# Kernel optimization log

Hardware: AMD Instinct MI355X
Metric: run time of the kernel (lower is better)

The kernel has to match this reference:

```python
import jax, jax.numpy as jnp
import numpy as np
import math

D_MODEL = 1024
EMB_DIM = 33
BANDS = (EMB_DIM - 1) // 2  # 16
FAST_DECAY_PCT = 0.3
SLOW_DECAY_PCT = 1.5
TARGET = 0.01
MOD_SHIFT = 0.0


def setup_inputs() -> dict:
    key = jax.random.key(0)
    ks = jax.random.split(key, 11)
    B, L = 2, 8192
    order = 64
    return {
        "x": jax.random.normal(ks[0], (B, D_MODEL, L), dtype=jnp.float32),
        "L": L,
        "lin_in_w": jax.random.normal(ks[1], (EMB_DIM, order), dtype=jnp.float32) * 0.1,
        "lin_in_b": jax.random.normal(ks[2], (order,), dtype=jnp.float32) * 0.1,
        "freq": jnp.ones((1, order), dtype=jnp.float32),  # Sin freq param, w=1
        "inner1_w": jax.random.normal(ks[3], (order, order), dtype=jnp.float32) * 0.1,
        "inner1_b": jax.random.normal(ks[4], (order,), dtype=jnp.float32) * 0.1,
        "inner2_w": jax.random.normal(ks[5], (order, order), dtype=jnp.float32) * 0.1,
        "inner2_b": jax.random.normal(ks[6], (order,), dtype=jnp.float32) * 0.1,
        "out_w": jax.random.normal(ks[7], (order, D_MODEL), dtype=jnp.float32) * 0.1,
        "D": jax.random.normal(ks[8], (D_MODEL,), dtype=jnp.float32),
    }


def _pos_emb(L):
    # ComplexExponentialPositionalEmbedding buffers (constants)
    t = jnp.linspace(0.0, 1.0, L, dtype=jnp.float32)[:, None]          # [L, 1]
    t_rescaled = jnp.linspace(0.0, L - 1, L, dtype=jnp.float32)[:, None]
    w = 2.0 * math.pi * t_rescaled / L                                  # [L, 1]
    f = jnp.linspace(1e-4, BANDS - 1, BANDS, dtype=jnp.float32)[None, :]
    theta = f * w                                                       # [L, bands]
    # z = exp(-1j * theta): real = cos(theta), imag = -sin(theta)
    z = jnp.concatenate([t, jnp.cos(theta), -jnp.sin(theta)], axis=-1)  # [L, emb_dim]
    return z, t


def reference(x, L, lin_in_w, lin_in_b, freq, inner1_w, inner1_b, inner2_w, inner2_b, out_w, D):
    # --- implicit filter MLP (Sin activations share one freq param) ---
    z, t = _pos_emb(L)
    h = jnp.sin(freq * (z @ lin_in_w + lin_in_b))
    h = jnp.sin(freq * (h @ inner1_w + inner1_b))
    h = jnp.sin(freq * (h @ inner2_w + inner2_b))
    h = h @ out_w                                                # [L, d_model]

    # --- exponential modulation ---
    max_decay = math.log(TARGET) / FAST_DECAY_PCT
    min_decay = math.log(TARGET) / SLOW_DECAY_PCT
    deltas = jnp.linspace(min_decay, max_decay, D_MODEL, dtype=jnp.float32)[None, :]
    decay = jnp.exp(-t * jnp.abs(deltas))                        # [L, d_model]
    h = h * (decay + MOD_SHIFT)

    k = h.T                                                      # [d_model, L]

    # --- FFT causal long convolution ---
    fft_size = 2 * L
    k_f = jnp.fft.rfft(k, n=fft_size) / fft_size                 # [d_model, L+1]
    u_f = jnp.fft.rfft(x, n=fft_size)                            # [B, d_model, L+1]
    y = jnp.fft.irfft(u_f * k_f, n=fft_size, norm="forward")[..., :L]
    out = y + x * D[:, None]                                     # bias skip connection
    return out.astype(x.dtype)
```

## Files before the change

### kernel.cpp

```cpp
#include <hip/hip_runtime.h>

#define D_MODEL 1024
#define LSEQ    8192
#define NC      8192
#define PI_F    3.14159265358979323846f
#define TWO_PI_OVER_N 3.8349519697141029e-4f
#define R2F  0.70710678118654752440f
#define C18F 0.92387953251128675613f
#define S18F 0.38268343236508977173f

__device__ __forceinline__ int sw(int p) { return p ^ ((p >> 7) & 15) ^ ((p >> 3) & 7); }
__device__ __forceinline__ int rev13(int x) { return (int)(__brev((unsigned)x) >> 19); }
__device__ __forceinline__ float2 cmulf(float2 a, float2 b) {
    return make_float2(a.x*b.x - a.y*b.y, a.x*b.y + a.y*b.x);
}

__device__ __forceinline__ void bf_dif(float2& a, float2& b, float c, float s) {
    float tx = a.x - b.x, ty = a.y - b.y;
    a.x += b.x; a.y += b.y;
    b.x = tx*c - ty*s; b.y = tx*s + ty*c;
}
__device__ __forceinline__ void bf_dif1(float2& a, float2& b) {
    float tx = a.x - b.x, ty = a.y - b.y;
    a.x += b.x; a.y += b.y;
    b.x = tx; b.y = ty;
}
__device__ __forceinline__ void bf_dif_mi(float2& a, float2& b) {
    float tx = a.x - b.x, ty = a.y - b.y;
    a.x += b.x; a.y += b.y;
    b.x = ty; b.y = -tx;
}
__device__ __forceinline__ void bf_dit(float2& a, float2& b, float c, float s) {
    float bx = b.x*c - b.y*s, by = b.x*s + b.y*c;
    b.x = a.x - bx; b.y = a.y - by;
    a.x += bx; a.y += by;
}
__device__ __forceinline__ void bf_dit1(float2& a, float2& b) {
    float bx = b.x, by = b.y;
    b.x = a.x - bx; b.y = a.y - by;
    a.x += bx; a.y += by;
}
__device__ __forceinline__ void bf_dit_pi(float2& a, float2& b) {
    float bx = -b.y, by = b.x;
    b.x = a.x - bx; b.y = a.y - by;
    a.x += bx; a.y += by;
}
__device__ __forceinline__ void bf_dit_a(float2& a, float2 b, float c, float s) {
    a.x += b.x*c - b.y*s; a.y += b.x*s + b.y*c;
}

template<int H>
__device__ __forceinline__ void fwd_pass8(float2* s, int tid) {
    const float astep = -PI_F / (float)H;
    #pragma unroll 1
    for (int gg = 0; gg < 4; ++gg) {
        int gi   = tid + gg * 256;
        int q    = gi & (H/4 - 1);
        int base = (gi - q) * 8 + q;
        float2 v[8];
        #pragma unroll
        for (int m = 0; m < 8; ++m) v[m] = s[sw(base + m*(H/4))];
        float a = astep * (float)q;
        float c1,s1,c2,s2,c4,s4;
        __sincosf(a,     &s1, &c1);
        __sincosf(a+a,   &s2, &c2);
        __sincosf(4.f*a, &s4, &c4);
        bf_dif(v[0], v[4], c1, s1);
        bf_dif(v[1], v[5], R2F*(c1+s1), R2F*(s1-c1));
        bf_dif(v[2], v[6], s1, -c1);
        bf_dif(v[3], v[7], R2F*(s1-c1), -R2F*(c1+s1));
        bf_dif(v[0], v[2], c2, s2);  bf_dif(v[4], v[6], c2, s2);
        bf_dif(v[1], v[3], s2, -c2); bf_dif(v[5], v[7], s2, -c2);
        bf_dif(v[0], v[1], c4, s4); bf_dif(v[2], v[3], c4, s4);
        bf_dif(v[4], v[5], c4, s4); bf_dif(v[6], v[7], c4, s4);
        #pragma unroll
        for (int m = 0; m < 8; ++m) s[sw(base + m*(H/4))] = v[m];
    }
}

__device__ __forceinline__ void dif16(float2* v) {
    bf_dif1 (v[0], v[8]);
    bf_dif  (v[1], v[9],   C18F, -S18F);
    bf_dif  (v[2], v[10],  R2F,  -R2F);
    bf_dif  (v[3], v[11],  S18F, -C18F);
    bf_dif_mi(v[4], v[12]);
    bf_dif  (v[5], v[13], -S18F, -C18F);
    bf_dif  (v[6], v[14], -R2F,  -R2F);
    bf_dif  (v[7], v[15], -C18F, -S18F);
    bf_dif1 (v[0], v[4]);              bf_dif1 (v[8],  v[12]);
    bf_dif  (v[1], v[5],  R2F, -R2F);  bf_dif  (v[9],  v[13],  R2F, -R2F);
    bf_dif_mi(v[2], v[6]);             bf_dif_mi(v[10], v[14]);
    bf_dif  (v[3], v[7], -R2F, -R2F);  bf_dif  (v[11], v[15], -R2F, -R2F);
    bf_dif1 (v[0], v[2]); bf_dif1 (v[4], v[6]); bf_dif1 (v[8], v[10]); bf_dif1 (v[12], v[14]);
    bf_dif_mi(v[1], v[3]); bf_dif_mi(v[5], v[7]); bf_dif_mi(v[9], v[11]); bf_dif_mi(v[13], v[15]);
    bf_dif1(v[0], v[1]); bf_dif1(v[2], v[3]);  bf_dif1(v[4], v[5]);  bf_dif1(v[6], v[7]);
    bf_dif1(v[8], v[9]); bf_dif1(v[10],v[11]); bf_dif1(v[12],v[13]); bf_dif1(v[14],v[15]);
}

__device__ __forceinline__ void fwd_fft(float2* s, int tid, const float2* __restrict__ g) {
    {
        const float astep = -PI_F / 4096.0f;
        #pragma unroll 1
        for (int gg = 0; gg < 4; ++gg) {
            int q = tid + gg * 256;
            float2 v[8];
            #pragma unroll
            for (int m = 0; m < 4; ++m) v[m] = g[q + m*1024];
            float a = astep * (float)q;
            float c1,s1,c2,s2,c4,s4;
            __sincosf(a,     &s1, &c1);
            __sincosf(a+a,   &s2, &c2);
            __sincosf(4.f*a, &s4, &c4);
            float wc, ws;
            wc = c1;            ws = s1;             v[4] = make_float2(v[0].x*wc - v[0].y*ws, v[0].x*ws + v[0].y*wc);
            wc = R2F*(c1+s1);   ws = R2F*(s1-c1);    v[5] = make_float2(v[1].x*wc - v[1].y*ws, v[1].x*ws + v[1].y*wc);
            wc = s1;            ws = -c1;            v[6] = make_float2(v[2].x*wc - v[2].y*ws, v[2].x*ws + v[2].y*wc);
            wc = R2F*(s1-c1);   ws = -R2F*(c1+s1);   v[7] = make_float2(v[3].x*wc - v[3].y*ws, v[3].x*ws + v[3].y*wc);
            bf_dif(v[0], v[2], c2, s2);  bf_dif(v[4], v[6], c2, s2);
            bf_dif(v[1], v[3], s2, -c2); bf_dif(v[5], v[7], s2, -c2);
            bf_dif(v[0], v[1], c4, s4); bf_dif(v[2], v[3], c4, s4);
            bf_dif(v[4], v[5], c4, s4); bf_dif(v[6], v[7], c4, s4);
            #pragma unroll
            for (int m = 0; m < 8; ++m) s[sw(q + m*1024)] = v[m];
        }
    }
    __syncthreads();
    fwd_pass8<512>(s, tid);
    __syncthreads();
    fwd_pass8<64>(s, tid);
    __syncthreads();
    #pragma unroll 1
    for (int gg = 0; gg < 2; ++gg) {
        int base = (tid + gg * 256) << 4;
        float2 v[16];
        #pragma unroll
        for (int m = 0; m < 16; ++m) v[m] = s[sw(base + m)];
        dif16(v);
        #pragma unroll
        for (int m = 0; m < 16; ++m) s[sw(base + m)] = v[m];
    }
}

__device__ __forceinline__ void dit16(float2* v) {
    bf_dit1(v[0], v[1]); bf_dit1(v[2], v[3]);  bf_dit1(v[4], v[5]);  bf_dit1(v[6], v[7]);
    bf_dit1(v[8], v[9]); bf_dit1(v[10],v[11]); bf_dit1(v[12],v[13]); bf_dit1(v[14],v[15]);
    bf_dit1 (v[0], v[2]); bf_dit_pi(v[1], v[3]);
    bf_dit1 (v[4], v[6]); bf_dit_pi(v[5], v[7]);
    bf_dit1 (v[8], v[10]); bf_dit_pi(v[9], v[11]);
    bf_dit1 (v[12],v[14]); bf_dit_pi(v[13],v[15]);
    bf_dit1 (v[0], v[4]);             bf_dit1 (v[8],  v[12]);
    bf_dit  (v[1], v[5],  R2F, R2F);  bf_dit  (v[9],  v[13],  R2F, R2F);
    bf_dit_pi(v[2], v[6]);            bf_dit_pi(v[10], v[14]);
    bf_dit  (v[3], v[7], -R2F, R2F);  bf_dit  (v[11], v[15], -R2F, R2F);
    bf_dit1 (v[0], v[8]);
    bf_dit  (v[1], v[9],   C18F, S18F);
    bf_dit  (v[2], v[10],  R2F,  R2F);
    bf_dit  (v[3], v[11],  S18F, C18F);
    bf_dit_pi(v[4], v[12]);
    bf_dit  (v[5], v[13], -S18F, C18F);
    bf_dit  (v[6], v[14], -R2F,  R2F);
    bf_dit  (v[7], v[15], -C18F, S18F);
}

template<int H>
__device__ __forceinline__ void inv_pass8(float2* s, int tid) {
    const float bstep = PI_F / (float)(4*H);
    #pragma unroll 1
    for (int gg = 0; gg < 4; ++gg) {
        int gi   = tid + gg * 256;
        int q    = gi & (H - 1);
        int base = (gi - q) * 8 + q;
        float2 v[8];
        #pragma unroll
        for (int m = 0; m < 8; ++m) v[m] = s[sw(base + m*H)];
        float bb = bstep * (float)q;
        float cb,sb,c2,s2,c4,s4;
        __sincosf(bb,      &sb, &cb);
        __sincosf(bb+bb,   &s2, &c2);
        __sincosf(4.f*bb,  &s4, &c4);
        bf_dit(v[0],v[1],c4,s4); bf_dit(v[2],v[3],c4,s4);
        bf_dit(v[4],v[5],c4,s4); bf_dit(v[6],v[7],c4,s4);
        bf_dit(v[0],v[2], c2,s2);  bf_dit(v[4],v[6], c2,s2);
        bf_dit(v[1],v[3],-s2,c2);  bf_dit(v[5],v[7],-s2,c2);
        bf_dit(v[0],v[4],  cb, sb);
        bf_dit(v[1],v[5],  R2F*(cb-sb), R2F*(sb+cb));
        bf_dit(v[2],v[6], -sb, cb);
        bf_dit(v[3],v[7], -R2F*(sb+cb), R2F*(cb-sb));
        #pragma unroll
        for (int m = 0; m < 8; ++m) s[sw(base + m*H)] = v[m];
    }
}

__device__ __forceinline__ void inv_last_out(const float2* s, int tid,
                                             const float2* __restrict__ xv,
                                             float2* __restrict__ ov, float Dd) {
    const float bstep = PI_F / 4096.0f;
    #pragma unroll 1
    for (int gg = 0; gg < 4; ++gg) {
        int q = tid + gg * 256;
        float2 v[8];
        #pragma unroll
        for (int m = 0; m < 8; ++m) v[m] = s[sw(q + m*1024)];
        float bb = bstep * (float)q;
        float cb,sb,c2,s2,c4,s4;
        __sincosf(bb,      &sb, &cb);
        __sincosf(bb+bb,   &s2, &c2);
        __sincosf(4.f*bb,  &s4, &c4);
        bf_dit(v[0],v[1],c4,s4); bf_dit(v[2],v[3],c4,s4);
        bf_dit(v[4],v[5],c4,s4); bf_dit(v[6],v[7],c4,s4);
        bf_dit(v[0],v[2], c2,s2);  bf_dit(v[4],v[6], c2,s2);
        bf_dit(v[1],v[3],-s2,c2);  bf_dit(v[5],v[7],-s2,c2);
        bf_dit_a(v[0], v[4],  cb, sb);
        bf_dit_a(v[1], v[5],  R2F*(cb-sb), R2F*(sb+cb));
        bf_dit_a(v[2], v[6], -sb, cb);
        bf_dit_a(v[3], v[7], -R2F*(sb+cb), R2F*(cb-sb));
        #pragma unroll
        for (int m = 0; m < 4; ++m) {
            int n = q + m*1024;
            float2 xx = xv[n];
            ov[n] = make_float2(v[m].x + xx.x * Dd, v[m].y + xx.y * Dd);
        }
    }
}

__global__ void __launch_bounds__(256) hyena_filter_k(
    const float* __restrict__ W1, const float* __restrict__ b1,
    const float* __restrict__ freq,
    const float* __restrict__ W2, const float* __restrict__ b2,
    const float* __restrict__ W3, const float* __restrict__ b3,
    const float* __restrict__ Wout,
    float* __restrict__ kout)
{
    __shared__ float zbuf[64][35];
    __shared__ float abuf[64][65];
    __shared__ float bbuf[64][65];

    const int tid = threadIdx.x;
    const int pbase = blockIdx.x * 64;

    for (int idx = tid; idx < 64 * 33; idx += 256) {
        int p = idx & 63, e = idx >> 6;
        int gp = pbase + p;
        float w = 7.6699039394282907e-4f * (float)gp;
        float val;
        if (e == 0) {
            val = (float)gp / 8191.0f;
        } else if (e < 17) {
            float f = 1.0e-4f + (float)(e - 1) * ((15.0f - 1.0e-4f) / 15.0f);
            val = cosf(f * w);
        } else {
            float f = 1.0e-4f + (float)(e - 17) * ((15.0f - 1.0e-4f) / 15.0f);
            val = -sinf(f * w);
        }
        zbuf[p][e] = val;
    }
    __syncthreads();

    const int p  = tid & 63;
    const int g4 = __builtin_amdgcn_readfirstlane(tid >> 6);
    const int ob = g4 * 16;

    {
        float acc[16];
        #pragma unroll
        for (int oo = 0; oo < 16; ++oo) acc[oo] = b1[ob + oo];
        #pragma unroll
        for (int e = 0; e < 33; ++e) {
            float ae = zbuf[p][e];
            const float* wr = W1 + e * 64 + ob;
            #pragma unroll
            for (int oo = 0; oo < 16; ++oo) acc[oo] += ae * wr[oo];
        }
        #pragma unroll
        for (int oo = 0; oo < 16; ++oo) abuf[p][ob + oo] = __sinf(freq[ob + oo] * acc[oo]);
    }
    __syncthreads();
    {
        float acc[16];
        #pragma unroll
        for (int oo = 0; oo < 16; ++oo) acc[oo] = b2[ob + oo];
        #pragma unroll
        for (int e = 0; e < 64; ++e) {
            float ae = abuf[p][e];
            const float* wr = W2 + e * 64 + ob;
            #pragma unroll
            for (int oo = 0; oo < 16; ++oo) acc[oo] += ae * wr[oo];
        }
        #pragma unroll
        for (int oo = 0; oo < 16; ++oo) bbuf[p][ob + oo] = __sinf(freq[ob + oo] * acc[oo]);
    }
    __syncthreads();
    {
        float acc[16];
        #pragma unroll
        for (int oo = 0; oo < 16; ++oo) acc[oo] = b3[ob + oo];
        #pragma unroll
        for (int e = 0; e < 64; ++e) {
            float ae = bbuf[p][e];
            const float* wr = W3 + e * 64 + ob;
            #pragma unroll
            for (int oo = 0; oo < 16; ++oo) acc[oo] += ae * wr[oo];
        }
        #pragma unroll
        for (int oo = 0; oo < 16; ++oo) abuf[p][ob + oo] = __sinf(freq[ob + oo] * acc[oo]);
    }
    __syncthreads();

    {
        const int gp = pbase + p;
        const float t = (float)gp / 8191.0f;
        const float mind  = -3.0701134573253940f;
        const float dstep = -0.012004353694331942f;
        const int dd0 = blockIdx.y * 128 + g4 * 32;

        float acc[32];
        #pragma unroll
        for (int ii = 0; ii < 32; ++ii) acc[ii] = 0.0f;

        #pragma unroll 4
        for (int o = 0; o < 64; ++o) {
            float h = abuf[p][o];
            const float* wr = Wout + o * 1024 + dd0;
            #pragma unroll
            for (int ii = 0; ii < 32; ++ii) acc[ii] += h * wr[ii];
        }
        #pragma unroll
        for (int ii = 0; ii < 32; ++ii) {
            int dd = dd0 + ii;
            float delta = fabsf(mind + dstep * (float)dd);
            kout[(size_t)dd * LSEQ + gp] = acc[ii] * __expf(-t * delta);
        }
    }
}

__global__ void __launch_bounds__(256) hyena_conv_k(
    const float* __restrict__ x, const float* kin,
    const float* __restrict__ Dvec, float* out)
{
    __shared__ float2 s[NC];
    const int tid = threadIdx.x;
    const int d = blockIdx.x;
    const float Dd = Dvec[d];
    const float invN = 1.0f / 16384.0f;

    fwd_fft(s, tid, (const float2*)(kin + (size_t)d * LSEQ));
    __syncthreads();

    float2 Kk[16], Km[16];
    #pragma unroll
    for (int j = 0; j < 16; ++j) {
        int k = tid + j * 256;
        if (k == 0) {
            float2 C0 = s[0];
            Kk[0] = make_float2((C0.x + C0.y) * invN, (C0.x - C0.y) * invN);
            float2 C = s[1];
            Km[0] = make_float2(C.x * invN, -C.y * invN);
        } else {
            int m = NC - k;
            float2 Ck = s[sw(rev13(k))], Cm = s[sw(rev13(m))];
            float sn, cs;
            __sincosf(TWO_PI_OVER_N * (float)k, &sn, &cs);
            float2 E = make_float2(Ck.x + Cm.x, Ck.y - Cm.y);
            float2 O = make_float2(Ck.x - Cm.x, Ck.y + Cm.y);
            float2 WO = make_float2(O.x * cs + O.y * sn, -O.x * sn + O.y * cs);
            float2 T = make_float2(-WO.y, WO.x);
            Kk[j] = make_float2(0.5f * invN * (E.x - T.x),  0.5f * invN * (E.y - T.y));
            Km[j] = make_float2(0.5f * invN * (E.x + T.x), -0.5f * invN * (E.y + T.y));
        }
    }

    for (int b = 0; b < 2; ++b) {
        __syncthreads();
        const size_t base = ((size_t)b * D_MODEL + d) * LSEQ;
        fwd_fft(s, tid, (const float2*)(x + base));
        __syncthreads();

        #pragma unroll
        for (int j = 0; j < 16; ++j) {
            int k = tid + j * 256;
            if (k == 0) {
                float2 C0 = s[0];
                float U0 = C0.x + C0.y, UN = C0.x - C0.y;
                float Y0 = U0 * Kk[0].x, YN = UN * Kk[0].y;
                s[0] = make_float2(Y0 + YN, Y0 - YN);
                float2 C = s[1];
                float2 U = make_float2(C.x, -C.y);
                float2 Y = cmulf(U, Km[0]);
                s[1] = make_float2(2.0f * Y.x, -2.0f * Y.y);
            } else {
                int m = NC - k;
                int pk = sw(rev13(k)), pm = sw(rev13(m));
                float2 Ck = s[pk], Cm = s[pm];
                float sn, cs;
                __sincosf(TWO_PI_OVER_N * (float)k, &sn, &cs);
                float2 E = make_float2(Ck.x + Cm.x, Ck.y - Cm.y);
                float2 O = make_float2(Ck.x - Cm.x, Ck.y + Cm.y);
                float2 WO = make_float2(O.x * cs + O.y * sn, -O.x * sn + O.y * cs);
                float2 T = make_float2(-WO.y, WO.x);
                float2 Uk = make_float2(0.5f * (E.x - T.x),  0.5f * (E.y - T.y));
                float2 Um = make_float2(0.5f * (E.x + T.x), -0.5f * (E.y + T.y));
                float2 Yk = cmulf(Uk, Kk[j]);
                float2 Ym = cmulf(Um, Km[j]);
                float2 P = make_float2(Yk.x + Ym.x, Yk.y - Ym.y);
                float2 Q = make_float2(Yk.x - Ym.x, Yk.y + Ym.y);
                float2 CQ = make_float2(Q.x * cs - Q.y * sn, Q.x * sn + Q.y * cs);
                float2 T2 = make_float2(-CQ.y, CQ.x);
                s[pk] = make_float2(P.x + T2.x, P.y + T2.y);
                s[pm] = make_float2(P.x - T2.x, -(P.y - T2.y));
            }
        }
        __syncthreads();

        #pragma unroll 1
        for (int gg = 0; gg < 2; ++gg) {
            int b16 = (tid + gg * 256) << 4;
            float2 v[16];
            #pragma unroll
            for (int m = 0; m < 16; ++m) v[m] = s[sw(b16 + m)];
            dit16(v);
            #pragma unroll
            for (int m = 0; m < 16; ++m) s[sw(b16 + m)] = v[m];
        }
        __syncthreads();
        inv_pass8<16>(s, tid);
        __syncthreads();
        inv_pass8<128>(s, tid);
        __syncthreads();
        inv_last_out(s, tid, (const float2*)(x + base), (float2*)(out + base), Dd);
    }
}

extern "C" void kernel_launch(void* const* d_in, const int* in_sizes, int n_in,
                              void* d_out, int out_size, void* d_ws, size_t ws_size,
                              hipStream_t stream) {
    (void)in_sizes; (void)n_in; (void)out_size; (void)d_ws; (void)ws_size;
    const float* x    = (const float*)d_in[0];
    const float* W1   = (const float*)d_in[2];
    const float* b1   = (const float*)d_in[3];
    const float* freq = (const float*)d_in[4];
    const float* W2   = (const float*)d_in[5];
    const float* b2   = (const float*)d_in[6];
    const float* W3   = (const float*)d_in[7];
    const float* b3   = (const float*)d_in[8];
    const float* Wout = (const float*)d_in[9];
    const float* Dv   = (const float*)d_in[10];
    float* out = (float*)d_out;

    float* kbuf = out;

    hipLaunchKernelGGL(hyena_filter_k, dim3(128, 8), dim3(256), 0, stream,
                       W1, b1, freq, W2, b2, W3, b3, Wout, kbuf);
    hipLaunchKernelGGL(hyena_conv_k, dim3(1024), dim3(256), 0, stream,
                       x, kbuf, Dv, out);
}
```

Before: 349.9 us.

## Use 1024-thread blocks for FFT conv and restructure filter MLP loops

The FFT convolution kernel moves from 256 to 1024 threads per block, so each thread handles one radix-8 group per pass instead of looping four times. Each thread now keeps only four kernel-spectrum pairs in registers instead of sixteen. The filter kernel drops the shared positional-embedding buffer and computes cos/sin on the fly, and it stages hidden activations into small register chunks. The aim is more parallelism and latency hiding inside each FFT, at the cost of idle threads in the radix-16 stages (only 512 active) and fewer blocks resident per CU.

Measured after the change: 723.9 us. 2.07x slower.

```diff
diff --git a/kernel.cpp b/kernel.cpp
--- a/kernel.cpp
+++ b/kernel.cpp
@@ -49,33 +49,30 @@
     a.x += b.x*c - b.y*s; a.y += b.x*s + b.y*c;
 }
 
+
 template<int H>
 __device__ __forceinline__ void fwd_pass8(float2* s, int tid) {
     const float astep = -PI_F / (float)H;
-    #pragma unroll 1
-    for (int gg = 0; gg < 4; ++gg) {
-        int gi   = tid + gg * 256;
-        int q    = gi & (H/4 - 1);
-        int base = (gi - q) * 8 + q;
-        float2 v[8];
-        #pragma unroll
-        for (int m = 0; m < 8; ++m) v[m] = s[sw(base + m*(H/4))];
-        float a = astep * (float)q;
-        float c1,s1,c2,s2,c4,s4;
-        __sincosf(a,     &s1, &c1);
-        __sincosf(a+a,   &s2, &c2);
-        __sincosf(4.f*a, &s4, &c4);
-        bf_dif(v[0], v[4], c1, s1);
-        bf_dif(v[1], v[5], R2F*(c1+s1), R2F*(s1-c1));
-        bf_dif(v[2], v[6], s1, -c1);
-        bf_dif(v[3], v[7], R2F*(s1-c1), -R2F*(c1+s1));
-        bf_dif(v[0], v[2], c2, s2);  bf_dif(v[4], v[6], c2, s2);
-        bf_dif(v[1], v[3], s2, -c2); bf_dif(v[5], v[7], s2, -c2);
-        bf_dif(v[0], v[1], c4, s4); bf_dif(v[2], v[3], c4, s4);
-        bf_dif(v[4], v[5], c4, s4); bf_dif(v[6], v[7], c4, s4);
-        #pragma unroll
-        for (int m = 0; m < 8; ++m) s[sw(base + m*(H/4))] = v[m];
-    }
+    int q    = tid & (H/4 - 1);
+    int base = (tid - q) * 8 + q;
+    float2 v[8];
+    #pragma unroll
+    for (int m = 0; m < 8; ++m) v[m] = s[sw(base + m*(H/4))];
+    float a = astep * (float)q;
+    float c1,s1,c2,s2,c4,s4;
+    __sincosf(a,     &s1, &c1);
+    __sincosf(a+a,   &s2, &c2);
+    __sincosf(4.f*a, &s4, &c4);
+    bf_dif(v[0], v[4], c1, s1);
+    bf_dif(v[1], v[5], R2F*(c1+s1), R2F*(s1-c1));
+    bf_dif(v[2], v[6], s1, -c1);
+    bf_dif(v[3], v[7], R2F*(s1-c1), -R2F*(c1+s1));
+    bf_dif(v[0], v[2], c2, s2);  bf_dif(v[4], v[6], c2, s2);
+    bf_dif(v[1], v[3], s2, -c2); bf_dif(v[5], v[7], s2, -c2);
+    bf_dif(v[0], v[1], c4, s4); bf_dif(v[2], v[3], c4, s4);
+    bf_dif(v[4], v[5], c4, s4); bf_dif(v[6], v[7], c4, s4);
+    #pragma unroll
+    for (int m = 0; m < 8; ++m) s[sw(base + m*(H/4))] = v[m];
 }
 
 __device__ __forceinline__ void dif16(float2* v) {
@@ -100,38 +97,34 @@
 __device__ __forceinline__ void fwd_fft(float2* s, int tid, const float2* __restrict__ g) {
     {
         const float astep = -PI_F / 4096.0f;
-        #pragma unroll 1
-        for (int gg = 0; gg < 4; ++gg) {
-            int q = tid + gg * 256;
-            float2 v[8];
-            #pragma unroll
-            for (int m = 0; m < 4; ++m) v[m] = g[q + m*1024];
-            float a = astep * (float)q;
-            float c1,s1,c2,s2,c4,s4;
-            __sincosf(a,     &s1, &c1);
-            __sincosf(a+a,   &s2, &c2);
-            __sincosf(4.f*a, &s4, &c4);
-            float wc, ws;
-            wc = c1;            ws = s1;             v[4] = make_float2(v[0].x*wc - v[0].y*ws, v[0].x*ws + v[0].y*wc);
-            wc = R2F*(c1+s1);   ws = R2F*(s1-c1);    v[5] = make_float2(v[1].x*wc - v[1].y*ws, v[1].x*ws + v[1].y*wc);
-            wc = s1;            ws = -c1;            v[6] = make_float2(v[2].x*wc - v[2].y*ws, v[2].x*ws + v[2].y*wc);
-            wc = R2F*(s1-c1);   ws = -R2F*(c1+s1);   v[7] = make_float2(v[3].x*wc - v[3].y*ws, v[3].x*ws + v[3].y*wc);
-            bf_dif(v[0], v[2], c2, s2);  bf_dif(v[4], v[6], c2, s2);
-            bf_dif(v[1], v[3], s2, -c2); bf_dif(v[5], v[7], s2, -c2);
-            bf_dif(v[0], v[1], c4, s4); bf_dif(v[2], v[3], c4, s4);
-            bf_dif(v[4], v[5], c4, s4); bf_dif(v[6], v[7], c4, s4);
-            #pragma unroll
-            for (int m = 0; m < 8; ++m) s[sw(q + m*1024)] = v[m];
-        }
+        int q = tid;
+        float2 v[8];
+        #pragma unroll
+        for (int m = 0; m < 4; ++m) v[m] = g[q + m*1024];
+        float a = astep * (float)q;
+        float c1,s1,c2,s2,c4,s4;
+        __sincosf(a,     &s1, &c1);
+        __sincosf(a+a,   &s2, &c2);
+        __sincosf(4.f*a, &s4, &c4);
+        float wc, ws;
+        wc = c1;            ws = s1;             v[4] = make_float2(v[0].x*wc - v[0].y*ws, v[0].x*ws + v[0].y*wc);
+        wc = R2F*(c1+s1);   ws = R2F*(s1-c1);    v[5] = make_float2(v[1].x*wc - v[1].y*ws, v[1].x*ws + v[1].y*wc);
+        wc = s1;            ws = -c1;            v[6] = make_float2(v[2].x*wc - v[2].y*ws, v[2].x*ws + v[2].y*wc);
+        wc = R2F*(s1-c1);   ws = -R2F*(c1+s1);   v[7] = make_float2(v[3].x*wc - v[3].y*ws, v[3].x*ws + v[3].y*wc);
+        bf_dif(v[0], v[2], c2, s2);  bf_dif(v[4], v[6], c2, s2);
+        bf_dif(v[1], v[3], s2, -c2); bf_dif(v[5], v[7], s2, -c2);
+        bf_dif(v[0], v[1], c4, s4); bf_dif(v[2], v[3], c4, s4);
+        bf_dif(v[4], v[5], c4, s4); bf_dif(v[6], v[7], c4, s4);
+        #pragma unroll
+        for (int m = 0; m < 8; ++m) s[sw(q + m*1024)] = v[m];
     }
     __syncthreads();
     fwd_pass8<512>(s, tid);
     __syncthreads();
     fwd_pass8<64>(s, tid);
     __syncthreads();
-    #pragma unroll 1
-    for (int gg = 0; gg < 2; ++gg) {
-        int base = (tid + gg * 256) << 4;
+    if (tid < 512) {
+        int base = tid << 4;
         float2 v[16];
         #pragma unroll
         for (int m = 0; m < 16; ++m) v[m] = s[sw(base + m)];
@@ -165,65 +158,94 @@
 template<int H>
 __device__ __forceinline__ void inv_pass8(float2* s, int tid) {
     const float bstep = PI_F / (float)(4*H);
-    #pragma unroll 1
-    for (int gg = 0; gg < 4; ++gg) {
-        int gi   = tid + gg * 256;
-        int q    = gi & (H - 1);
-        int base = (gi - q) * 8 + q;
-        float2 v[8];
-        #pragma unroll
-        for (int m = 0; m < 8; ++m) v[m] = s[sw(base + m*H)];
-        float bb = bstep * (float)q;
-        float cb,sb,c2,s2,c4,s4;
-        __sincosf(bb,      &sb, &cb);
-        __sincosf(bb+bb,   &s2, &c2);
-        __sincosf(4.f*bb,  &s4, &c4);
-        bf_dit(v[0],v[1],c4,s4); bf_dit(v[2],v[3],c4,s4);
-        bf_dit(v[4],v[5],c4,s4); bf_dit(v[6],v[7],c4,s4);
-        bf_dit(v[0],v[2], c2,s2);  bf_dit(v[4],v[6], c2,s2);
-        bf_dit(v[1],v[3],-s2,c2);  bf_dit(v[5],v[7],-s2,c2);
-        bf_dit(v[0],v[4],  cb, sb);
-        bf_dit(v[1],v[5],  R2F*(cb-sb), R2F*(sb+cb));
-        bf_dit(v[2],v[6], -sb, cb);
-        bf_dit(v[3],v[7], -R2F*(sb+cb), R2F*(cb-sb));
-        #pragma unroll
-        for (int m = 0; m < 8; ++m) s[sw(base + m*H)] = v[m];
-    }
+    int q    = tid & (H - 1);
+    int base = (tid - q) * 8 + q;
+    float2 v[8];
+    #pragma unroll
+    for (int m = 0; m < 8; ++m) v[m] = s[sw(base + m*H)];
+    float bb = bstep * (float)q;
+    float cb,sb,c2,s2,c4,s4;
+    __sincosf(bb,      &sb, &cb);
+    __sincosf(bb+bb,   &s2, &c2);
+    __sincosf(4.f*bb,  &s4, &c4);
+    bf_dit(v[0],v[1],c4,s4); bf_dit(v[2],v[3],c4,s4);
+    bf_dit(v[4],v[5],c4,s4); bf_dit(v[6],v[7],c4,s4);
+    bf_dit(v[0],v[2], c2,s2);  bf_dit(v[4],v[6], c2,s2);
+    bf_dit(v[1],v[3],-s2,c2);  bf_dit(v[5],v[7],-s2,c2);
+    bf_dit(v[0],v[4],  cb, sb);
+    bf_dit(v[1],v[5],  R2F*(cb-sb), R2F*(sb+cb));
+    bf_dit(v[2],v[6], -sb, cb);
+    bf_dit(v[3],v[7], -R2F*(sb+cb), R2F*(cb-sb));
+    #pragma unroll
+    for (int m = 0; m < 8; ++m) s[sw(base + m*H)] = v[m];
 }
 
 __device__ __forceinline__ void inv_last_out(const float2* s, int tid,
                                              const float2* __restrict__ xv,
                                              float2* __restrict__ ov, float Dd) {
     const float bstep = PI_F / 4096.0f;
-    #pragma unroll 1
-    for (int gg = 0; gg < 4; ++gg) {
-        int q = tid + gg * 256;
-        float2 v[8];
-        #pragma unroll
-        for (int m = 0; m < 8; ++m) v[m] = s[sw(q + m*1024)];
-        float bb = bstep * (float)q;
-        float cb,sb,c2,s2,c4,s4;
-        __sincosf(bb,      &sb, &cb);
-        __sincosf(bb+bb,   &s2, &c2);
-        __sincosf(4.f*bb,  &s4, &c4);
-        bf_dit(v[0],v[1],c4,s4); bf_dit(v[2],v[3],c4,s4);
-        bf_dit(v[4],v[5],c4,s4); bf_dit(v[6],v[7],c4,s4);
-        bf_dit(v[0],v[2], c2,s2);  bf_dit(v[4],v[6], c2,s2);
-        bf_dit(v[1],v[3],-s2,c2);  bf_dit(v[5],v[7],-s2,c2);
-        bf_dit_a(v[0], v[4],  cb, sb);
-        bf_dit_a(v[1], v[5],  R2F*(cb-sb), R2F*(sb+cb));
-        bf_dit_a(v[2], v[6], -sb, cb);
-        bf_dit_a(v[3], v[7], -R2F*(sb+cb), R2F*(cb-sb));
-        #pragma unroll
-        for (int m = 0; m < 4; ++m) {
-            int n = q + m*1024;
-            float2 xx = xv[n];
-            ov[n] = make_float2(v[m].x + xx.x * Dd, v[m].y + xx.y * Dd);
-        }
-    }
-}
-
-__global__ void __launch_bounds__(256) hyena_filter_k(
+    int q = tid;
+    float2 v[8];
+    #pragma unroll
+    for (int m = 0; m < 8; ++m) v[m] = s[sw(q + m*1024)];
+    float bb = bstep * (float)q;
+    float cb,sb,c2,s2,c4,s4;
+    __sincosf(bb,      &sb, &cb);
+    __sincosf(bb+bb,   &s2, &c2);
+    __sincosf(4.f*bb,  &s4, &c4);
+    bf_dit(v[0],v[1],c4,s4); bf_dit(v[2],v[3],c4,s4);
+    bf_dit(v[4],v[5],c4,s4); bf_dit(v[6],v[7],c4,s4);
+    bf_dit(v[0],v[2], c2,s2);  bf_dit(v[4],v[6], c2,s2);
+    bf_dit(v[1],v[3],-s2,c2);  bf_dit(v[5],v[7],-s2,c2);
+    bf_dit_a(v[0], v[4],  cb, sb);
+    bf_dit_a(v[1], v[5],  R2F*(cb-sb), R2F*(sb+cb));
+    bf_dit_a(v[2], v[6], -sb, cb);
+    bf_dit_a(v[3], v[7], -R2F*(sb+cb), R2F*(cb-sb));
+    #pragma unroll
+    for (int m = 0; m < 4; ++m) {
+        int n = q + m*1024;
+        float2 xx = xv[n];
+        ov[n] = make_float2(v[m].x + xx.x * Dd, v[m].y + xx.y * Dd);
+    }
+}
+
+__device__ __forceinline__ void k_unpack(const float2* s, int k, float invN,
+                                         float2& Kkj, float2& Kmj) {
+    int m = NC - k;
+    float2 Ck = s[sw(rev13(k))], Cm = s[sw(rev13(m))];
+    float sn, cs;
+    __sincosf(TWO_PI_OVER_N * (float)k, &sn, &cs);
+    float2 E = make_float2(Ck.x + Cm.x, Ck.y - Cm.y);
+    float2 O = make_float2(Ck.x - Cm.x, Ck.y + Cm.y);
+    float2 WO = make_float2(O.x * cs + O.y * sn, -O.x * sn + O.y * cs);
+    float2 T = make_float2(-WO.y, WO.x);
+    Kkj = make_float2(0.5f * invN * (E.x - T.x),  0.5f * invN * (E.y - T.y));
+    Kmj = make_float2(0.5f * invN * (E.x + T.x), -0.5f * invN * (E.y + T.y));
+}
+
+__device__ __forceinline__ void mul_one(float2* s, int k, float2 Kkj, float2 Kmj) {
+    int m = NC - k;
+    int pk = sw(rev13(k)), pm = sw(rev13(m));
+    float2 Ck = s[pk], Cm = s[pm];
+    float sn, cs;
+    __sincosf(TWO_PI_OVER_N * (float)k, &sn, &cs);
+    float2 E = make_float2(Ck.x + Cm.x, Ck.y - Cm.y);
+    float2 O = make_float2(Ck.x - Cm.x, Ck.y + Cm.y);
+    float2 WO = make_float2(O.x * cs + O.y * sn, -O.x * sn + O.y * cs);
+    float2 T = make_float2(-WO.y, WO.x);
+    float2 Uk = make_float2(0.5f * (E.x - T.x),  0.5f * (E.y - T.y));
+    float2 Um = make_float2(0.5f * (E.x + T.x), -0.5f * (E.y + T.y));
+    float2 Yk = cmulf(Uk, Kkj);
+    float2 Ym = cmulf(Um, Kmj);
+    float2 P = make_float2(Yk.x + Ym.x, Yk.y - Ym.y);
+    float2 Q = make_float2(Yk.x - Ym.x, Yk.y + Ym.y);
+    float2 CQ = make_float2(Q.x * cs - Q.y * sn, Q.x * sn + Q.y * cs);
+    float2 T2 = make_float2(-CQ.y, CQ.x);
+    s[pk] = make_float2(P.x + T2.x, P.y + T2.y);
+    s[pm] = make_float2(P.x - T2.x, -(P.y - T2.y));
+}
+
+__global__ void __launch_bounds__(256, 4) hyena_filter_k(
     const float* __restrict__ W1, const float* __restrict__ b1,
     const float* __restrict__ freq,
     const float* __restrict__ W2, const float* __restrict__ b2,
@@ -231,42 +253,39 @@
     const float* __restrict__ Wout,
     float* __restrict__ kout)
 {
-    __shared__ float zbuf[64][35];
     __shared__ float abuf[64][65];
     __shared__ float bbuf[64][65];
 
     const int tid = threadIdx.x;
     const int pbase = blockIdx.x * 64;
-
-    for (int idx = tid; idx < 64 * 33; idx += 256) {
-        int p = idx & 63, e = idx >> 6;
-        int gp = pbase + p;
-        float w = 7.6699039394282907e-4f * (float)gp;
-        float val;
-        if (e == 0) {
-            val = (float)gp / 8191.0f;
-        } else if (e < 17) {
-            float f = 1.0e-4f + (float)(e - 1) * ((15.0f - 1.0e-4f) / 15.0f);
-            val = cosf(f * w);
-        } else {
-            float f = 1.0e-4f + (float)(e - 17) * ((15.0f - 1.0e-4f) / 15.0f);
-            val = -sinf(f * w);
-        }
-        zbuf[p][e] = val;
-    }
-    __syncthreads();
-
     const int p  = tid & 63;
     const int g4 = __builtin_amdgcn_readfirstlane(tid >> 6);
     const int ob = g4 * 16;
+    const int gp = pbase + p;
+    const float w = 7.6699039394282907e-4f * (float)gp;
 
     {
         float acc[16];
         #pragma unroll
         for (int oo = 0; oo < 16; ++oo) acc[oo] = b1[ob + oo];
-        #pragma unroll
-        for (int e = 0; e < 33; ++e) {
-            float ae = zbuf[p][e];
+        {
+            float ae = (float)gp / 8191.0f;
+            const float* wr = W1 + ob;
+            #pragma unroll
+            for (int oo = 0; oo < 16; ++oo) acc[oo] += ae * wr[oo];
+        }
+        #pragma unroll
+        for (int e = 1; e < 17; ++e) {
+            float f = 1.0e-4f + (float)(e - 1) * ((15.0f - 1.0e-4f) / 15.0f);
+            float ae = cosf(f * w);
+            const float* wr = W1 + e * 64 + ob;
+            #pragma unroll
+            for (int oo = 0; oo < 16; ++oo) acc[oo] += ae * wr[oo];
+        }
+        #pragma unroll
+        for (int e = 17; e < 33; ++e) {
+            float f = 1.0e-4f + (float)(e - 17) * ((15.0f - 1.0e-4f) / 15.0f);
+            float ae = -sinf(f * w);
             const float* wr = W1 + e * 64 + ob;
             #pragma unroll
             for (int oo = 0; oo < 16; ++oo) acc[oo] += ae * wr[oo];
@@ -279,12 +298,17 @@
         float acc[16];
         #pragma unroll
         for (int oo = 0; oo < 16; ++oo) acc[oo] = b2[ob + oo];
-        #pragma unroll
-        for (int e = 0; e < 64; ++e) {
-            float ae = abuf[p][e];
-            const float* wr = W2 + e * 64 + ob;
-            #pragma unroll
-            for (int oo = 0; oo < 16; ++oo) acc[oo] += ae * wr[oo];
+        #pragma unroll 1
+        for (int eb = 0; eb < 8; ++eb) {
+            float hreg[8];
+            #pragma unroll
+            for (int j = 0; j < 8; ++j) hreg[j] = abuf[p][eb * 8 + j];
+            #pragma unroll
+            for (int j = 0; j < 8; ++j) {
+                const float* wr = W2 + (eb * 8 + j) * 64 + ob;
+                #pragma unroll
+                for (int oo = 0; oo < 16; ++oo) acc[oo] += hreg[j] * wr[oo];
+            }
         }
         #pragma unroll
         for (int oo = 0; oo < 16; ++oo) bbuf[p][ob + oo] = __sinf(freq[ob + oo] * acc[oo]);
@@ -294,12 +318,17 @@
         float acc[16];
         #pragma unroll
         for (int oo = 0; oo < 16; ++oo) acc[oo] = b3[ob + oo];
-        #pragma unroll
-        for (int e = 0; e < 64; ++e) {
-            float ae = bbuf[p][e];
-            const float* wr = W3 + e * 64 + ob;
-            #pragma unroll
-            for (int oo = 0; oo < 16; ++oo) acc[oo] += ae * wr[oo];
+        #pragma unroll 1
+        for (int eb = 0; eb < 8; ++eb) {
+            float hreg[8];
+            #pragma unroll
+            for (int j = 0; j < 8; ++j) hreg[j] = bbuf[p][eb * 8 + j];
+            #pragma unroll
+            for (int j = 0; j < 8; ++j) {
+                const float* wr = W3 + (eb * 8 + j) * 64 + ob;
+                #pragma unroll
+                for (int oo = 0; oo < 16; ++oo) acc[oo] += hreg[j] * wr[oo];
+            }
         }
         #pragma unroll
         for (int oo = 0; oo < 16; ++oo) abuf[p][ob + oo] = __sinf(freq[ob + oo] * acc[oo]);
@@ -307,7 +336,6 @@
     __syncthreads();
 
     {
-        const int gp = pbase + p;
         const float t = (float)gp / 8191.0f;
         const float mind  = -3.0701134573253940f;
         const float dstep = -0.012004353694331942f;
@@ -317,12 +345,17 @@
         #pragma unroll
         for (int ii = 0; ii < 32; ++ii) acc[ii] = 0.0f;
 
-        #pragma unroll 4
-        for (int o = 0; o < 64; ++o) {
-            float h = abuf[p][o];
-            const float* wr = Wout + o * 1024 + dd0;
-            #pragma unroll
-            for (int ii = 0; ii < 32; ++ii) acc[ii] += h * wr[ii];
+        #pragma unroll 1
+        for (int eb = 0; eb < 16; ++eb) {
+            float hreg[4];
+            #pragma unroll
+            for (int j = 0; j < 4; ++j) hreg[j] = abuf[p][eb * 4 + j];
+            #pragma unroll
+            for (int j = 0; j < 4; ++j) {
+                const float* wr = Wout + (eb * 4 + j) * 1024 + dd0;
+                #pragma unroll
+                for (int ii = 0; ii < 32; ++ii) acc[ii] += hreg[j] * wr[ii];
+            }
         }
         #pragma unroll
         for (int ii = 0; ii < 32; ++ii) {
@@ -333,7 +366,7 @@
     }
 }
 
-__global__ void __launch_bounds__(256) hyena_conv_k(
+__global__ void __launch_bounds__(1024) hyena_conv_k(
     const float* __restrict__ x, const float* kin,
     const float* __restrict__ Dvec, float* out)
 {
@@ -346,28 +379,18 @@
     fwd_fft(s, tid, (const float2*)(kin + (size_t)d * LSEQ));
     __syncthreads();
 
-    float2 Kk[16], Km[16];
-    #pragma unroll
-    for (int j = 0; j < 16; ++j) {
-        int k = tid + j * 256;
-        if (k == 0) {
-            float2 C0 = s[0];
-            Kk[0] = make_float2((C0.x + C0.y) * invN, (C0.x - C0.y) * invN);
-            float2 C = s[1];
-            Km[0] = make_float2(C.x * invN, -C.y * invN);
-        } else {
-            int m = NC - k;
-            float2 Ck = s[sw(rev13(k))], Cm = s[sw(rev13(m))];
-            float sn, cs;
-            __sincosf(TWO_PI_OVER_N * (float)k, &sn, &cs);
-            float2 E = make_float2(Ck.x + Cm.x, Ck.y - Cm.y);
-            float2 O = make_float2(Ck.x - Cm.x, Ck.y + Cm.y);
-            float2 WO = make_float2(O.x * cs + O.y * sn, -O.x * sn + O.y * cs);
-            float2 T = make_float2(-WO.y, WO.x);
-            Kk[j] = make_float2(0.5f * invN * (E.x - T.x),  0.5f * invN * (E.y - T.y));
-            Km[j] = make_float2(0.5f * invN * (E.x + T.x), -0.5f * invN * (E.y + T.y));
-        }
-    }
+    float2 Kk0, Kk1, Kk2, Kk3, Km0, Km1, Km2, Km3;
+    if (tid == 0) {
+        float2 C0 = s[0];
+        Kk0 = make_float2((C0.x + C0.y) * invN, (C0.x - C0.y) * invN);
+        float2 C = s[1];
+        Km0 = make_float2(C.x * invN, -C.y * invN);
+    } else {
+        k_unpack(s, tid, invN, Kk0, Km0);
+    }
+    k_unpack(s, tid + 1024, invN, Kk1, Km1);
+    k_unpack(s, tid + 2048, invN, Kk2, Km2);
+    k_unpack(s, tid + 3072, invN, Kk3, Km3);
 
     for (int b = 0; b < 2; ++b) {
         __syncthreads();
@@ -375,45 +398,25 @@
         fwd_fft(s, tid, (const float2*)(x + base));
         __syncthreads();
 
-        #pragma unroll
-        for (int j = 0; j < 16; ++j) {
-            int k = tid + j * 256;
-            if (k == 0) {
-                float2 C0 = s[0];
-                float U0 = C0.x + C0.y, UN = C0.x - C0.y;
-                float Y0 = U0 * Kk[0].x, YN = UN * Kk[0].y;
-                s[0] = make_float2(Y0 + YN, Y0 - YN);
-                float2 C = s[1];
-                float2 U = make_float2(C.x, -C.y);
-                float2 Y = cmulf(U, Km[0]);
-                s[1] = make_float2(2.0f * Y.x, -2.0f * Y.y);
-            } else {
-                int m = NC - k;
-                int pk = sw(rev13(k)), pm = sw(rev13(m));
-                float2 Ck = s[pk], Cm = s[pm];
-                float sn, cs;
-                __sincosf(TWO_PI_OVER_N * (float)k, &sn, &cs);
-                float2 E = make_float2(Ck.x + Cm.x, Ck.y - Cm.y);
-                float2 O = make_float2(Ck.x - Cm.x, Ck.y + Cm.y);
-                float2 WO = make_float2(O.x * cs + O.y * sn, -O.x * sn + O.y * cs);
-                float2 T = make_float2(-WO.y, WO.x);
-                float2 Uk = make_float2(0.5f * (E.x - T.x),  0.5f * (E.y - T.y));
-                float2 Um = make_float2(0.5f * (E.x + T.x), -0.5f * (E.y + T.y));
-                float2 Yk = cmulf(Uk, Kk[j]);
-                float2 Ym = cmulf(Um, Km[j]);
-                float2 P = make_float2(Yk.x + Ym.x, Yk.y - Ym.y);
-                float2 Q = make_float2(Yk.x - Ym.x, Yk.y + Ym.y);
-                float2 CQ = make_float2(Q.x * cs - Q.y * sn, Q.x * sn + Q.y * cs);
-                float2 T2 = make_float2(-CQ.y, CQ.x);
-                s[pk] = make_float2(P.x + T2.x, P.y + T2.y);
-                s[pm] = make_float2(P.x - T2.x, -(P.y - T2.y));
-            }
-        }
-        __syncthreads();
-
-        #pragma unroll 1
-        for (int gg = 0; gg < 2; ++gg) {
-            int b16 = (tid + gg * 256) << 4;
+        if (tid == 0) {
+            float2 C0 = s[0];
+            float U0 = C0.x + C0.y, UN = C0.x - C0.y;
+            float Y0 = U0 * Kk0.x, YN = UN * Kk0.y;
+            s[0] = make_float2(Y0 + YN, Y0 - YN);
+            float2 C = s[1];
+            float2 U = make_float2(C.x, -C.y);
+            float2 Y = cmulf(U, Km0);
+            s[1] = make_float2(2.0f * Y.x, -2.0f * Y.y);
+        } else {
+            mul_one(s, tid, Kk0, Km0);
+        }
+        mul_one(s, tid + 1024, Kk1, Km1);
+        mul_one(s, tid + 2048, Kk2, Km2);
+        mul_one(s, tid + 3072, Kk3, Km3);
+        __syncthreads();
+
+        if (tid < 512) {
+            int b16 = tid << 4;
             float2 v[16];
             #pragma unroll
             for (int m = 0; m < 16; ++m) v[m] = s[sw(b16 + m)];
@@ -450,6 +453,6 @@
 
     hipLaunchKernelGGL(hyena_filter_k, dim3(128, 8), dim3(256), 0, stream,
                        W1, b1, freq, W2, b2, W3, b3, Wout, kbuf);
-    hipLaunchKernelGGL(hyena_conv_k, dim3(1024), dim3(256), 0, stream,
+    hipLaunchKernelGGL(hyena_conv_k, dim3(1024), dim3(1024), 0, stream,
                        x, kbuf, Dv, out);
 }
```
